# Performance work log

Hardware: AMD Instinct MI355X
Metric: run time of the kernel (lower is better)

## Reference

```python
import jax, jax.numpy as jnp
import numpy as np

H = 4  # heads
L = 2  # num_layers


def _segment_softmax(alpha, seg, num_segments):
    # alpha: [E, H], seg: [E] destination node ids
    m = jax.ops.segment_max(alpha, seg, num_segments=num_segments)  # [N, H]
    m = jnp.where(jnp.isfinite(m), m, 0.0)
    ex = jnp.exp(alpha - m[seg])
    s = jax.ops.segment_sum(ex, seg, num_segments=num_segments)  # [N, H]
    return ex / (s[seg] + 1e-16)


def _conv(x, src, dst, edge_weight, edge_attr, wq, wk, wv, we, g, b):
    # x: [N, D]; edge_attr: [E, D]; one WePredConv layer (eval mode, no dropout)
    N, D = x.shape
    C = D // H
    q = (x @ wq).reshape(N, H, C)
    k = (x @ wk).reshape(N, H, C)
    v = (x @ wv).reshape(N, H, C)
    e = (edge_attr @ we).reshape(-1, H, C)
    alpha = (q[dst] + k[src] + e).sum(-1) / jnp.sqrt(jnp.float32(C))  # [E, H]
    alpha = alpha + g[None, :] * edge_weight[:, None]
    alpha = jax.nn.leaky_relu(alpha, negative_slope=0.2)
    alpha = _segment_softmax(alpha, dst, N)
    msg = v[src] * alpha[:, :, None]  # [E, H, C]
    out = jax.ops.segment_sum(msg, dst, num_segments=N).reshape(N, H * C)
    return out + b


def setup_inputs() -> dict:
    key = jax.random.key(0)
    ks = jax.random.split(key, 12)
    N, E, D, F, R = 50000, 400000, 128, 256, 200
    sc = 0.08  # ~xavier scale
    return {
        "entity": jnp.arange(N, dtype=jnp.int32),
        "edge_index": jax.random.randint(ks[0], (2, E), 0, N, dtype=jnp.int32),
        "edge_type": jax.random.randint(ks[1], (E,), 0, R, dtype=jnp.int32),
        "edge_weight": jax.random.uniform(ks[2], (E,), dtype=jnp.float32),
        "ent_table": jax.random.normal(ks[3], (N, F), dtype=jnp.float32),
        "proj_w": jax.random.normal(ks[4], (F, D), dtype=jnp.float32) * sc,
        "proj_b": jnp.zeros((D,), dtype=jnp.float32),
        "rel_emb": jax.random.normal(ks[5], (R, D), dtype=jnp.float32) * sc,
        "Wq": jax.random.normal(ks[6], (L, D, D), dtype=jnp.float32) * sc,
        "Wk": jax.random.normal(ks[7], (L, D, D), dtype=jnp.float32) * sc,
        "Wv": jax.random.normal(ks[8], (L, D, D), dtype=jnp.float32) * sc,
        "We": jax.random.normal(ks[9], (L, D, D), dtype=jnp.float32) * sc,
        "gate": jnp.ones((L, H), dtype=jnp.float32),
        "conv_bias": jnp.zeros((L, D), dtype=jnp.float32),
    }


def reference(entity, edge_index, edge_type, edge_weight, ent_table, proj_w,
              proj_b, rel_emb, Wq, Wk, Wv, We, gate, conv_bias):
    src, dst = edge_index[0], edge_index[1]
    x = ent_table[entity] @ proj_w + proj_b          # [N, D]
    edge_attr = rel_emb[edge_type]                   # [E, D]
    for l in range(L):
        x = _conv(x, src, dst, edge_weight, edge_attr,
                  Wq[l], Wk[l], Wv[l], We[l], gate[l], conv_bias[l])
        if l != L - 1:
            x = jax.nn.elu(x)
    return x
```

## Files before the change

kernel.cpp:

```cpp
#include <hip/hip_runtime.h>

#define HD 4
#define DD 128
#define CC 32
#define SCAN_B 64
#define SCAN_T 256

typedef float  f32x4  __attribute__((ext_vector_type(4)));
typedef short  short8v __attribute__((ext_vector_type(8)));

__device__ __forceinline__ unsigned short f2bf(float x) {
    unsigned u = __float_as_uint(x);
    return (unsigned short)((u + 0x7FFFu + ((u >> 16) & 1u)) >> 16);
}
__device__ __forceinline__ float bf2f(unsigned short h) {
    return __uint_as_float((unsigned)h << 16);
}

__global__ __launch_bounds__(256) void prep_kernel(
    const float* __restrict__ Wq, const float* __restrict__ Wk,
    const float* __restrict__ We, const float* __restrict__ rel,
    float* __restrict__ Wqh, float* __restrict__ Wkh,
    float* __restrict__ esum, int R)
{
    __shared__ float WehS[2][DD][HD];
    int tid = threadIdx.x;
    for (int i = tid; i < 2 * DD * HD; i += 256) {
        int l = i / (DD * HD);
        int d = (i / HD) % DD;
        int h = i % HD;
        const float* bq = Wq + ((size_t)l * DD + d) * DD + h * CC;
        const float* bk = Wk + ((size_t)l * DD + d) * DD + h * CC;
        const float* be = We + ((size_t)l * DD + d) * DD + h * CC;
        float sq = 0.f, sk = 0.f, se = 0.f;
        for (int c = 0; c < CC; ++c) { sq += bq[c]; sk += bk[c]; se += be[c]; }
        Wqh[i] = sq; Wkh[i] = sk; WehS[l][d][h] = se;
    }
    __syncthreads();
    for (int i = tid; i < 2 * R * HD; i += 256) {
        int l = i / (R * HD);
        int r = (i / HD) % R;
        int h = i % HD;
        const float* rp = rel + (size_t)r * DD;
        float a = 0.f;
        for (int d = 0; d < DD; ++d) a += rp[d] * WehS[l][d][h];
        esum[i] = a;
    }
}

__global__ __launch_bounds__(256) void prep_bt(
    const float* __restrict__ pw, const float* __restrict__ Wv,
    unsigned short* __restrict__ btp_h, unsigned short* __restrict__ btp_l,
    unsigned short* __restrict__ btv_h, unsigned short* __restrict__ btv_l)
{
    int t = blockIdx.x * 256 + threadIdx.x;
    if (t < 128 * 256) {
        int col = t >> 8, k = t & 255;
        float v = pw[(size_t)k * DD + col];
        unsigned short h = f2bf(v);
        btp_h[(size_t)col * 256 + k] = h;
        btp_l[(size_t)col * 256 + k] = f2bf(v - bf2f(h));
    } else if (t < 128 * 256 + 2 * DD * DD) {
        int u = t - 128 * 256;
        int l = u >> 14;
        int r = u & 16383;
        int col = r >> 7, k = r & 127;
        float v = Wv[((size_t)l * DD + k) * DD + col];
        unsigned short h = f2bf(v);
        btv_h[((size_t)l * DD + col) * DD + k] = h;
        btv_l[((size_t)l * DD + col) * DD + k] = f2bf(v - bf2f(h));
    }
}

__global__ __launch_bounds__(256) void gemm_mfma(
    const float* __restrict__ A, const int* __restrict__ gather,
    const unsigned short* __restrict__ bth, const unsigned short* __restrict__ btl,
    const float* __restrict__ bias,
    const float* __restrict__ Wqh, const float* __restrict__ Wkh,
    float* __restrict__ C, float* __restrict__ qs, float* __restrict__ ks,
    int M, int K)
{
    __shared__ unsigned short Ah[64][40], Al[64][40];
    __shared__ unsigned short Bh[128][40], Bl[128][40];
    __shared__ float wq[DD * HD], wk[DD * HD];

    const int tid = threadIdx.x;
    const int wave = tid >> 6, lane = tid & 63;
    const int row0 = blockIdx.x * 64;

    if (qs) {
        for (int i = tid; i < DD * HD; i += 256) { wq[i] = Wqh[i]; wk[i] = Wkh[i]; }
    }

    const int sr = tid >> 3;
    const int sc = (tid & 7) * 4;
    int r1 = row0 + sr;      if (r1 >= M) r1 = M - 1;
    int r2 = row0 + sr + 32; if (r2 >= M) r2 = M - 1;
    const int g1 = gather ? gather[r1] : r1;
    const int g2 = gather ? gather[r2] : r2;
    const float* Ap0 = A + (size_t)g1 * K;
    const float* Ap1 = A + (size_t)g2 * K;

    const int bcol = tid & 127;
    const int bseg = (tid >> 7) * 16;
    const unsigned short* bhp = bth + (size_t)bcol * K;
    const unsigned short* blp = btl + (size_t)bcol * K;

    const int fr = lane & 15, fg = lane >> 4;

    f32x4 acc[8] = {};
    float qp0[4] = {}, qp1[4] = {}, kp0[4] = {}, kp1[4] = {};

    for (int k0 = 0; k0 < K; k0 += 32) {
        float4 a0 = *(const float4*)(Ap0 + k0 + sc);
        float4 a1 = *(const float4*)(Ap1 + k0 + sc);
        short8v bh0 = *(const short8v*)(bhp + k0 + bseg);
        short8v bh1 = *(const short8v*)(bhp + k0 + bseg + 8);
        short8v bl0 = *(const short8v*)(blp + k0 + bseg);
        short8v bl1 = *(const short8v*)(blp + k0 + bseg + 8);
        __syncthreads();
        {
            short4 h0, l0, h1, l1;
            unsigned short h;
            h = f2bf(a0.x); h0.x = (short)h; l0.x = (short)f2bf(a0.x - bf2f(h));
            h = f2bf(a0.y); h0.y = (short)h; l0.y = (short)f2bf(a0.y - bf2f(h));
            h = f2bf(a0.z); h0.z = (short)h; l0.z = (short)f2bf(a0.z - bf2f(h));
            h = f2bf(a0.w); h0.w = (short)h; l0.w = (short)f2bf(a0.w - bf2f(h));
            h = f2bf(a1.x); h1.x = (short)h; l1.x = (short)f2bf(a1.x - bf2f(h));
            h = f2bf(a1.y); h1.y = (short)h; l1.y = (short)f2bf(a1.y - bf2f(h));
            h = f2bf(a1.z); h1.z = (short)h; l1.z = (short)f2bf(a1.z - bf2f(h));
            h = f2bf(a1.w); h1.w = (short)h; l1.w = (short)f2bf(a1.w - bf2f(h));
            *(short4*)&Ah[sr][sc]      = h0; *(short4*)&Al[sr][sc]      = l0;
            *(short4*)&Ah[sr + 32][sc] = h1; *(short4*)&Al[sr + 32][sc] = l1;
        }
        *(short8v*)&Bh[bcol][bseg]     = bh0;
        *(short8v*)&Bh[bcol][bseg + 8] = bh1;
        *(short8v*)&Bl[bcol][bseg]     = bl0;
        *(short8v*)&Bl[bcol][bseg + 8] = bl1;
        if (qs) {
            const float av0[4] = {a0.x, a0.y, a0.z, a0.w};
            const float av1[4] = {a1.x, a1.y, a1.z, a1.w};
#pragma unroll
            for (int i = 0; i < 4; ++i) {
                float4 qw = *(const float4*)&wq[(k0 + sc + i) * HD];
                float4 kw = *(const float4*)&wk[(k0 + sc + i) * HD];
                qp0[0] += av0[i] * qw.x; qp0[1] += av0[i] * qw.y;
                qp0[2] += av0[i] * qw.z; qp0[3] += av0[i] * qw.w;
                qp1[0] += av1[i] * qw.x; qp1[1] += av1[i] * qw.y;
                qp1[2] += av1[i] * qw.z; qp1[3] += av1[i] * qw.w;
                kp0[0] += av0[i] * kw.x; kp0[1] += av0[i] * kw.y;
                kp0[2] += av0[i] * kw.z; kp0[3] += av0[i] * kw.w;
                kp1[0] += av1[i] * kw.x; kp1[1] += av1[i] * kw.y;
                kp1[2] += av1[i] * kw.z; kp1[3] += av1[i] * kw.w;
            }
        }
        __syncthreads();
        short8v ah = *(const short8v*)&Ah[wave * 16 + fr][fg * 8];
        short8v al = *(const short8v*)&Al[wave * 16 + fr][fg * 8];
#pragma unroll
        for (int c = 0; c < 8; ++c) {
            short8v bh = *(const short8v*)&Bh[c * 16 + fr][fg * 8];
            short8v bl = *(const short8v*)&Bl[c * 16 + fr][fg * 8];
            acc[c] = __builtin_amdgcn_mfma_f32_16x16x32_bf16(ah, bh, acc[c], 0, 0, 0);
            acc[c] = __builtin_amdgcn_mfma_f32_16x16x32_bf16(ah, bl, acc[c], 0, 0, 0);
            acc[c] = __builtin_amdgcn_mfma_f32_16x16x32_bf16(al, bh, acc[c], 0, 0, 0);
        }
    }

    if (qs) {
#pragma unroll
        for (int off = 1; off < 8; off <<= 1) {
#pragma unroll
            for (int h = 0; h < 4; ++h) {
                qp0[h] += __shfl_xor(qp0[h], off, 64);
                qp1[h] += __shfl_xor(qp1[h], off, 64);
                kp0[h] += __shfl_xor(kp0[h], off, 64);
                kp1[h] += __shfl_xor(kp1[h], off, 64);
            }
        }
        if ((tid & 7) == 0) {
            int ra = row0 + sr, rb = row0 + sr + 32;
            if (ra < M) {
                *(float4*)&qs[(size_t)ra * HD] = make_float4(qp0[0], qp0[1], qp0[2], qp0[3]);
                *(float4*)&ks[(size_t)ra * HD] = make_float4(kp0[0], kp0[1], kp0[2], kp0[3]);
            }
            if (rb < M) {
                *(float4*)&qs[(size_t)rb * HD] = make_float4(qp1[0], qp1[1], qp1[2], qp1[3]);
                *(float4*)&ks[(size_t)rb * HD] = make_float4(kp1[0], kp1[1], kp1[2], kp1[3]);
            }
        }
    }

#pragma unroll
    for (int c = 0; c < 8; ++c) {
        float bv = bias ? bias[c * 16 + fr] : 0.f;
#pragma unroll
        for (int i = 0; i < 4; ++i) {
            int row = row0 + wave * 16 + fg * 4 + i;
            if (row < M) C[(size_t)row * DD + c * 16 + fr] = acc[c][i] + bv;
        }
    }
}

__global__ __launch_bounds__(256) void csr_count(
    const int* __restrict__ dstv, int* __restrict__ deg, int E)
{
    int t = blockIdx.x * 256 + threadIdx.x;
    if (t < E) atomicAdd(&deg[dstv[t]], 1);
}

__global__ __launch_bounds__(SCAN_T) void scan_partial(
    const int* __restrict__ deg, int* __restrict__ blksum, int N)
{
    __shared__ int red[SCAN_T];
    int chunk = (N + SCAN_B - 1) / SCAN_B;
    int b0 = blockIdx.x * chunk;
    int e0 = b0 + chunk; if (e0 > N) e0 = N;
    int s = 0;
    for (int i = b0 + threadIdx.x; i < e0; i += SCAN_T) s += deg[i];
    red[threadIdx.x] = s;
    __syncthreads();
    for (int off = SCAN_T / 2; off > 0; off >>= 1) {
        if (threadIdx.x < off) red[threadIdx.x] += red[threadIdx.x + off];
        __syncthreads();
    }
    if (threadIdx.x == 0) blksum[blockIdx.x] = red[0];
}

__global__ __launch_bounds__(64) void scan_blk(
    const int* __restrict__ blksum, int* __restrict__ blkoff)
{
    if (threadIdx.x == 0) {
        int acc = 0;
        for (int i = 0; i < SCAN_B; ++i) { blkoff[i] = acc; acc += blksum[i]; }
        blkoff[SCAN_B] = acc;
    }
}

__global__ __launch_bounds__(SCAN_T) void scan_final(
    const int* __restrict__ deg, const int* __restrict__ blkoff,
    int* __restrict__ row_ptr, int N)
{
    __shared__ int tsum[SCAN_T];
    int tid = threadIdx.x;
    int chunk = (N + SCAN_B - 1) / SCAN_B;
    int b0 = blockIdx.x * chunk;
    int e0 = b0 + chunk; if (e0 > N) e0 = N;
    int tchunk = (chunk + SCAN_T - 1) / SCAN_T;
    int tb = b0 + tid * tchunk;
    int te = tb + tchunk; if (te > e0) te = e0;
    int s = 0;
    for (int i = tb; i < te; ++i) s += deg[i];
    tsum[tid] = s;
    __syncthreads();
    for (int off = 1; off < SCAN_T; off <<= 1) {
        int v = (tid >= off) ? tsum[tid - off] : 0;
        __syncthreads();
        tsum[tid] += v;
        __syncthreads();
    }
    int base = blkoff[blockIdx.x] + ((tid == 0) ? 0 : tsum[tid - 1]);
    for (int i = tb; i < te; ++i) { row_ptr[i] = base; base += deg[i]; }
    if (blockIdx.x == SCAN_B - 1 && tid == SCAN_T - 1) row_ptr[N] = blkoff[SCAN_B];
}

__global__ __launch_bounds__(256) void csr_scatter(
    const int* __restrict__ srcv, const int* __restrict__ dstv,
    const int* __restrict__ etype, const float* __restrict__ ew,
    const int* __restrict__ row_ptr, int* __restrict__ cursor,
    int4* __restrict__ c_pack, int E)
{
    int e = blockIdx.x * 256 + threadIdx.x;
    if (e >= E) return;
    int d = dstv[e];
    int p = row_ptr[d] + atomicAdd(&cursor[d], 1);
    c_pack[p] = make_int4(srcv[e], etype[e], __float_as_int(ew[e]), 0);
}

__global__ __launch_bounds__(256) void fused_conv(
    const int* __restrict__ row_ptr, const int4* __restrict__ c_pack,
    const float* __restrict__ qs, const float* __restrict__ ks,
    const float* __restrict__ esum, const float* __restrict__ gate,
    const float* __restrict__ v, const float* __restrict__ bias,
    float* __restrict__ out, int N, int do_elu)
{
    int gw = (blockIdx.x * 256 + threadIdx.x) >> 6;
    int lane = threadIdx.x & 63;
    if (gw >= N) return;
    const int n = gw;
    const int beg = row_ptr[n], end = row_ptr[n + 1];
    const int c0 = lane * 2;
    const int h = lane >> 4;
    const float qh = qs[(size_t)n * HD + h];
    const float gh = gate[h];
    const float sc = 0.17677669529663687f;

    float num0 = 0.f, num1 = 0.f, den = 0.f;

    int j = beg;
    int4 p;
    if (j < end) p = c_pack[j];
    while (j < end) {
        int4 cur = p;
        ++j;
        if (j < end) p = c_pack[j];
        int s = cur.x, r = cur.y;
        float w = __int_as_float(cur.z);
        float kh = ks[(size_t)s * HD + h];
        float eh = esum[(size_t)r * HD + h];
        float2 vv = *(const float2*)&v[(size_t)s * DD + c0];
        float a = (qh + kh + eh) * sc + gh * w;
        a = a > 0.f ? a : 0.2f * a;
        float e = __expf(a);
        den += e;
        num0 = fmaf(e, vv.x, num0);
        num1 = fmaf(e, vv.y, num1);
    }

    float inv = 1.f / (den + 1e-16f);
    float r0 = num0 * inv + bias[c0];
    float r1 = num1 * inv + bias[c0 + 1];
    if (do_elu) {
        r0 = r0 > 0.f ? r0 : expm1f(r0);
        r1 = r1 > 0.f ? r1 : expm1f(r1);
    }
    *(float2*)&out[(size_t)n * DD + c0] = make_float2(r0, r1);
}

extern "C" void kernel_launch(void* const* d_in, const int* in_sizes, int n_in,
                              void* d_out, int out_size, void* d_ws, size_t ws_size,
                              hipStream_t stream)
{
    const int*   entity = (const int*)d_in[0];
    const int*   eidx   = (const int*)d_in[1];
    const int*   etype  = (const int*)d_in[2];
    const float* ew     = (const float*)d_in[3];
    const float* ent    = (const float*)d_in[4];
    const float* pw     = (const float*)d_in[5];
    const float* pb     = (const float*)d_in[6];
    const float* rel    = (const float*)d_in[7];
    const float* Wq     = (const float*)d_in[8];
    const float* Wk     = (const float*)d_in[9];
    const float* Wv     = (const float*)d_in[10];
    const float* We     = (const float*)d_in[11];
    const float* gate   = (const float*)d_in[12];
    const float* cb     = (const float*)d_in[13];

    const int N = in_sizes[0];
    const int E = in_sizes[2];
    const int F = in_sizes[4] / N;
    const int R = in_sizes[7] / DD;

    const int* srcv = eidx;
    const int* dstv = eidx + E;

    float* ws = (float*)d_ws;
    size_t o = 0;
    float* xbuf    = ws + o; o += (size_t)N * DD;
    float* vbuf    = ws + o; o += (size_t)N * DD;
    float* qs      = ws + o; o += (size_t)N * HD;
    float* ks      = ws + o; o += (size_t)N * HD;
    float* Wqh     = ws + o; o += 2 * DD * HD;
    float* Wkh     = ws + o; o += 2 * DD * HD;
    float* esum    = ws + o; o += (size_t)2 * R * HD;
    int*   deg     = (int*)(ws + o); o += N;
    int*   cursor  = (int*)(ws + o); o += N;
    int*   row_ptr = (int*)(ws + o); o += (size_t)N + 1;
    int*   blksum  = (int*)(ws + o); o += SCAN_B;
    int*   blkoff  = (int*)(ws + o); o += SCAN_B + 1;
    o = (o + 3) & ~(size_t)3;
    int4*  c_pack  = (int4*)(ws + o); o += (size_t)E * 4;
    unsigned short* btp_h = (unsigned short*)(ws + o); o += 128 * 256 / 2;
    unsigned short* btp_l = (unsigned short*)(ws + o); o += 128 * 256 / 2;
    unsigned short* btv_h = (unsigned short*)(ws + o); o += 2 * DD * DD / 2;
    unsigned short* btv_l = (unsigned short*)(ws + o); o += 2 * DD * DD / 2;

    prep_kernel<<<1, 256, 0, stream>>>(Wq, Wk, We, rel, Wqh, Wkh, esum, R);
    prep_bt<<<(128 * 256 + 2 * DD * DD + 255) / 256, 256, 0, stream>>>(
        pw, Wv, btp_h, btp_l, btv_h, btv_l);

    hipMemsetAsync(deg, 0, (size_t)2 * N * sizeof(int), stream);
    csr_count<<<(E + 255) / 256, 256, 0, stream>>>(dstv, deg, E);
    scan_partial<<<SCAN_B, SCAN_T, 0, stream>>>(deg, blksum, N);
    scan_blk<<<1, 64, 0, stream>>>(blksum, blkoff);
    scan_final<<<SCAN_B, SCAN_T, 0, stream>>>(deg, blkoff, row_ptr, N);
    csr_scatter<<<(E + 255) / 256, 256, 0, stream>>>(
        srcv, dstv, etype, ew, row_ptr, cursor, c_pack, E);

    const int gblk = (N + 63) / 64;
    gemm_mfma<<<gblk, 256, 0, stream>>>(
        ent, entity, btp_h, btp_l, pb, nullptr, nullptr,
        xbuf, nullptr, nullptr, N, F);

    const int fblk = (N + 3) / 4;
    for (int l = 0; l < 2; ++l) {
        gemm_mfma<<<gblk, 256, 0, stream>>>(
            xbuf, nullptr, btv_h + (size_t)l * DD * DD, btv_l + (size_t)l * DD * DD,
            nullptr, Wqh + l * DD * HD, Wkh + l * DD * HD,
            vbuf, qs, ks, N, DD);
        fused_conv<<<fblk, 256, 0, stream>>>(
            row_ptr, c_pack, qs, ks, esum + (size_t)l * R * HD,
            gate + l * HD, vbuf, cb + l * DD,
            (l == 0) ? xbuf : (float*)d_out, N, (l == 0) ? 1 : 0);
    }
}
```

Measured before the change: 265.7 us.

## Drop low-bf16 weight split and restage GEMM with 128-wide K chunks

```diff
diff --git a/kernel.cpp b/kernel.cpp
--- a/kernel.cpp
+++ b/kernel.cpp
@@ -6,7 +6,7 @@
 #define SCAN_B 64
 #define SCAN_T 256
 
-typedef float  f32x4  __attribute__((ext_vector_type(4)));
+typedef float  f32x4   __attribute__((ext_vector_type(4)));
 typedef short  short8v __attribute__((ext_vector_type(8)));
 
 __device__ __forceinline__ unsigned short f2bf(float x) {
@@ -50,38 +50,31 @@
 
 __global__ __launch_bounds__(256) void prep_bt(
     const float* __restrict__ pw, const float* __restrict__ Wv,
-    unsigned short* __restrict__ btp_h, unsigned short* __restrict__ btp_l,
-    unsigned short* __restrict__ btv_h, unsigned short* __restrict__ btv_l)
+    unsigned short* __restrict__ btp, unsigned short* __restrict__ btv)
 {
     int t = blockIdx.x * 256 + threadIdx.x;
     if (t < 128 * 256) {
         int col = t >> 8, k = t & 255;
-        float v = pw[(size_t)k * DD + col];
-        unsigned short h = f2bf(v);
-        btp_h[(size_t)col * 256 + k] = h;
-        btp_l[(size_t)col * 256 + k] = f2bf(v - bf2f(h));
+        btp[(size_t)col * 256 + k] = f2bf(pw[(size_t)k * DD + col]);
     } else if (t < 128 * 256 + 2 * DD * DD) {
         int u = t - 128 * 256;
         int l = u >> 14;
         int r = u & 16383;
         int col = r >> 7, k = r & 127;
-        float v = Wv[((size_t)l * DD + k) * DD + col];
-        unsigned short h = f2bf(v);
-        btv_h[((size_t)l * DD + col) * DD + k] = h;
-        btv_l[((size_t)l * DD + col) * DD + k] = f2bf(v - bf2f(h));
+        btv[((size_t)l * DD + col) * DD + k] = f2bf(Wv[((size_t)l * DD + k) * DD + col]);
     }
 }
 
 __global__ __launch_bounds__(256) void gemm_mfma(
     const float* __restrict__ A, const int* __restrict__ gather,
-    const unsigned short* __restrict__ bth, const unsigned short* __restrict__ btl,
-    const float* __restrict__ bias,
+    const unsigned short* __restrict__ bth, const float* __restrict__ bias,
     const float* __restrict__ Wqh, const float* __restrict__ Wkh,
     float* __restrict__ C, float* __restrict__ qs, float* __restrict__ ks,
     int M, int K)
 {
-    __shared__ unsigned short Ah[64][40], Al[64][40];
-    __shared__ unsigned short Bh[128][40], Bl[128][40];
+    __shared__ unsigned short AhL[4][4][64][8];
+    __shared__ unsigned short AlL[4][4][64][8];
+    __shared__ unsigned short BhL[4][8][64][8];
     __shared__ float wq[DD * HD], wk[DD * HD];
 
     const int tid = threadIdx.x;
@@ -92,101 +85,101 @@
         for (int i = tid; i < DD * HD; i += 256) { wq[i] = Wqh[i]; wk[i] = Wkh[i]; }
     }
 
-    const int sr = tid >> 3;
-    const int sc = (tid & 7) * 4;
-    int r1 = row0 + sr;      if (r1 >= M) r1 = M - 1;
-    int r2 = row0 + sr + 32; if (r2 >= M) r2 = M - 1;
-    const int g1 = gather ? gather[r1] : r1;
-    const int g2 = gather ? gather[r2] : r2;
-    const float* Ap0 = A + (size_t)g1 * K;
-    const float* Ap1 = A + (size_t)g2 * K;
-
-    const int bcol = tid & 127;
-    const int bseg = (tid >> 7) * 16;
-    const unsigned short* bhp = bth + (size_t)bcol * K;
-    const unsigned short* blp = btl + (size_t)bcol * K;
+    const int sr = tid >> 2;
+    const int sks = tid & 3;
+    int arow = row0 + sr; if (arow >= M) arow = M - 1;
+    const int ga = gather ? gather[arow] : arow;
+    const float* Ap = A + (size_t)ga * K + sks * 32;
+
+    const int bc = tid >> 1;
+    const int bh2 = (tid & 1) * 64;
+    const unsigned short* Bp = bth + (size_t)bc * K + bh2;
+    const int bct = bc >> 4, bfr = bc & 15;
 
     const int fr = lane & 15, fg = lane >> 4;
 
     f32x4 acc[8] = {};
-    float qp0[4] = {}, qp1[4] = {}, kp0[4] = {}, kp1[4] = {};
-
-    for (int k0 = 0; k0 < K; k0 += 32) {
-        float4 a0 = *(const float4*)(Ap0 + k0 + sc);
-        float4 a1 = *(const float4*)(Ap1 + k0 + sc);
-        short8v bh0 = *(const short8v*)(bhp + k0 + bseg);
-        short8v bh1 = *(const short8v*)(bhp + k0 + bseg + 8);
-        short8v bl0 = *(const short8v*)(blp + k0 + bseg);
-        short8v bl1 = *(const short8v*)(blp + k0 + bseg + 8);
+    float qp[4] = {}, kp[4] = {};
+
+    const int nch = K >> 7;
+    for (int ch = 0; ch < nch; ++ch) {
+        float4 a[8];
+#pragma unroll
+        for (int i = 0; i < 8; ++i) a[i] = *(const float4*)(Ap + ch * 128 + i * 4);
+        short8v b[8];
+#pragma unroll
+        for (int i = 0; i < 8; ++i) b[i] = *(const short8v*)(Bp + ch * 128 + i * 8);
+
+        if (ch) __syncthreads();
+
+        {
+            const int rt = sr >> 4, frr = sr & 15;
+#pragma unroll
+            for (int g = 0; g < 4; ++g) {
+                float vv[8] = {a[g*2].x, a[g*2].y, a[g*2].z, a[g*2].w,
+                               a[g*2+1].x, a[g*2+1].y, a[g*2+1].z, a[g*2+1].w};
+                short8v hv, lv;
+#pragma unroll
+                for (int j = 0; j < 8; ++j) {
+                    unsigned short h = f2bf(vv[j]);
+                    hv[j] = (short)h;
+                    lv[j] = (short)f2bf(vv[j] - bf2f(h));
+                }
+                *(short8v*)&AhL[rt][sks][g * 16 + frr][0] = hv;
+                *(short8v*)&AlL[rt][sks][g * 16 + frr][0] = lv;
+            }
+        }
+        if (qs) {
+#pragma unroll
+            for (int i = 0; i < 8; ++i) {
+                const float arr[4] = {a[i].x, a[i].y, a[i].z, a[i].w};
+#pragma unroll
+                for (int j = 0; j < 4; ++j) {
+                    int d = ch * 128 + sks * 32 + i * 4 + j;
+                    float4 qw = *(const float4*)&wq[d * HD];
+                    float4 kw = *(const float4*)&wk[d * HD];
+                    qp[0] += arr[j] * qw.x; qp[1] += arr[j] * qw.y;
+                    qp[2] += arr[j] * qw.z; qp[3] += arr[j] * qw.w;
+                    kp[0] += arr[j] * kw.x; kp[1] += arr[j] * kw.y;
+                    kp[2] += arr[j] * kw.z; kp[3] += arr[j] * kw.w;
+                }
+            }
+        }
+#pragma unroll
+        for (int g = 0; g < 8; ++g) {
+            int kk = bh2 + g * 8;
+            int ksb = kk >> 5, fgb = (kk & 31) >> 3;
+            *(short8v*)&BhL[ksb][bct][fgb * 16 + bfr][0] = b[g];
+        }
         __syncthreads();
-        {
-            short4 h0, l0, h1, l1;
-            unsigned short h;
-            h = f2bf(a0.x); h0.x = (short)h; l0.x = (short)f2bf(a0.x - bf2f(h));
-            h = f2bf(a0.y); h0.y = (short)h; l0.y = (short)f2bf(a0.y - bf2f(h));
-            h = f2bf(a0.z); h0.z = (short)h; l0.z = (short)f2bf(a0.z - bf2f(h));
-            h = f2bf(a0.w); h0.w = (short)h; l0.w = (short)f2bf(a0.w - bf2f(h));
-            h = f2bf(a1.x); h1.x = (short)h; l1.x = (short)f2bf(a1.x - bf2f(h));
-            h = f2bf(a1.y); h1.y = (short)h; l1.y = (short)f2bf(a1.y - bf2f(h));
-            h = f2bf(a1.z); h1.z = (short)h; l1.z = (short)f2bf(a1.z - bf2f(h));
-            h = f2bf(a1.w); h1.w = (short)h; l1.w = (short)f2bf(a1.w - bf2f(h));
-            *(short4*)&Ah[sr][sc]      = h0; *(short4*)&Al[sr][sc]      = l0;
-            *(short4*)&Ah[sr + 32][sc] = h1; *(short4*)&Al[sr + 32][sc] = l1;
-        }
-        *(short8v*)&Bh[bcol][bseg]     = bh0;
-        *(short8v*)&Bh[bcol][bseg + 8] = bh1;
-        *(short8v*)&Bl[bcol][bseg]     = bl0;
-        *(short8v*)&Bl[bcol][bseg + 8] = bl1;
-        if (qs) {
-            const float av0[4] = {a0.x, a0.y, a0.z, a0.w};
-            const float av1[4] = {a1.x, a1.y, a1.z, a1.w};
-#pragma unroll
-            for (int i = 0; i < 4; ++i) {
-                float4 qw = *(const float4*)&wq[(k0 + sc + i) * HD];
-                float4 kw = *(const float4*)&wk[(k0 + sc + i) * HD];
-                qp0[0] += av0[i] * qw.x; qp0[1] += av0[i] * qw.y;
-                qp0[2] += av0[i] * qw.z; qp0[3] += av0[i] * qw.w;
-                qp1[0] += av1[i] * qw.x; qp1[1] += av1[i] * qw.y;
-                qp1[2] += av1[i] * qw.z; qp1[3] += av1[i] * qw.w;
-                kp0[0] += av0[i] * kw.x; kp0[1] += av0[i] * kw.y;
-                kp0[2] += av0[i] * kw.z; kp0[3] += av0[i] * kw.w;
-                kp1[0] += av1[i] * kw.x; kp1[1] += av1[i] * kw.y;
-                kp1[2] += av1[i] * kw.z; kp1[3] += av1[i] * kw.w;
-            }
-        }
-        __syncthreads();
-        short8v ah = *(const short8v*)&Ah[wave * 16 + fr][fg * 8];
-        short8v al = *(const short8v*)&Al[wave * 16 + fr][fg * 8];
-#pragma unroll
-        for (int c = 0; c < 8; ++c) {
-            short8v bh = *(const short8v*)&Bh[c * 16 + fr][fg * 8];
-            short8v bl = *(const short8v*)&Bl[c * 16 + fr][fg * 8];
-            acc[c] = __builtin_amdgcn_mfma_f32_16x16x32_bf16(ah, bh, acc[c], 0, 0, 0);
-            acc[c] = __builtin_amdgcn_mfma_f32_16x16x32_bf16(ah, bl, acc[c], 0, 0, 0);
-            acc[c] = __builtin_amdgcn_mfma_f32_16x16x32_bf16(al, bh, acc[c], 0, 0, 0);
+
+#pragma unroll
+        for (int ksc = 0; ksc < 4; ++ksc) {
+            short8v ah = *(const short8v*)&AhL[wave][ksc][lane][0];
+            short8v al = *(const short8v*)&AlL[wave][ksc][lane][0];
+#pragma unroll
+            for (int c = 0; c < 8; ++c) {
+                short8v bh = *(const short8v*)&BhL[ksc][c][lane][0];
+                acc[c] = __builtin_amdgcn_mfma_f32_16x16x32_bf16(ah, bh, acc[c], 0, 0, 0);
+                acc[c] = __builtin_amdgcn_mfma_f32_16x16x32_bf16(al, bh, acc[c], 0, 0, 0);
+            }
         }
     }
 
     if (qs) {
 #pragma unroll
-        for (int off = 1; off < 8; off <<= 1) {
+        for (int off = 1; off < 4; off <<= 1) {
 #pragma unroll
             for (int h = 0; h < 4; ++h) {
-                qp0[h] += __shfl_xor(qp0[h], off, 64);
-                qp1[h] += __shfl_xor(qp1[h], off, 64);
-                kp0[h] += __shfl_xor(kp0[h], off, 64);
-                kp1[h] += __shfl_xor(kp1[h], off, 64);
-            }
-        }
-        if ((tid & 7) == 0) {
-            int ra = row0 + sr, rb = row0 + sr + 32;
-            if (ra < M) {
-                *(float4*)&qs[(size_t)ra * HD] = make_float4(qp0[0], qp0[1], qp0[2], qp0[3]);
-                *(float4*)&ks[(size_t)ra * HD] = make_float4(kp0[0], kp0[1], kp0[2], kp0[3]);
-            }
-            if (rb < M) {
-                *(float4*)&qs[(size_t)rb * HD] = make_float4(qp1[0], qp1[1], qp1[2], qp1[3]);
-                *(float4*)&ks[(size_t)rb * HD] = make_float4(kp1[0], kp1[1], kp1[2], kp1[3]);
+                qp[h] += __shfl_xor(qp[h], off, 64);
+                kp[h] += __shfl_xor(kp[h], off, 64);
+            }
+        }
+        if ((tid & 3) == 0) {
+            int row = row0 + sr;
+            if (row < M) {
+                *(float4*)&qs[(size_t)row * HD] = make_float4(qp[0], qp[1], qp[2], qp[3]);
+                *(float4*)&ks[(size_t)row * HD] = make_float4(kp[0], kp[1], kp[2], kp[3]);
             }
         }
     }
@@ -370,14 +363,12 @@
     int*   blkoff  = (int*)(ws + o); o += SCAN_B + 1;
     o = (o + 3) & ~(size_t)3;
     int4*  c_pack  = (int4*)(ws + o); o += (size_t)E * 4;
-    unsigned short* btp_h = (unsigned short*)(ws + o); o += 128 * 256 / 2;
-    unsigned short* btp_l = (unsigned short*)(ws + o); o += 128 * 256 / 2;
-    unsigned short* btv_h = (unsigned short*)(ws + o); o += 2 * DD * DD / 2;
-    unsigned short* btv_l = (unsigned short*)(ws + o); o += 2 * DD * DD / 2;
+    unsigned short* btp = (unsigned short*)(ws + o); o += 128 * 256 / 2;
+    unsigned short* btv = (unsigned short*)(ws + o); o += 2 * DD * DD / 2;
 
     prep_kernel<<<1, 256, 0, stream>>>(Wq, Wk, We, rel, Wqh, Wkh, esum, R);
     prep_bt<<<(128 * 256 + 2 * DD * DD + 255) / 256, 256, 0, stream>>>(
-        pw, Wv, btp_h, btp_l, btv_h, btv_l);
+        pw, Wv, btp, btv);
 
     hipMemsetAsync(deg, 0, (size_t)2 * N * sizeof(int), stream);
     csr_count<<<(E + 255) / 256, 256, 0, stream>>>(dstv, deg, E);
@@ -389,14 +380,14 @@
 
     const int gblk = (N + 63) / 64;
     gemm_mfma<<<gblk, 256, 0, stream>>>(
-        ent, entity, btp_h, btp_l, pb, nullptr, nullptr,
+        ent, entity, btp, pb, nullptr, nullptr,
         xbuf, nullptr, nullptr, N, F);
 
     const int fblk = (N + 3) / 4;
     for (int l = 0; l < 2; ++l) {
         gemm_mfma<<<gblk, 256, 0, stream>>>(
-            xbuf, nullptr, btv_h + (size_t)l * DD * DD, btv_l + (size_t)l * DD * DD,
-            nullptr, Wqh + l * DD * HD, Wkh + l * DD * HD,
+            xbuf, nullptr, btv + (size_t)l * DD * DD, nullptr,
+            Wqh + l * DD * HD, Wkh + l * DD * HD,
             vbuf, qs, ks, N, DD);
         fused_conv<<<fblk, 256, 0, stream>>>(
             row_ptr, c_pack, qs, ks, esum + (size_t)l * R * HD,
```

Measured after the change: 256.6 us. 3.4% less time.
